# Optimization experiments

Hardware: AMD Instinct MI355X
Metric: run time of the kernel (lower is better)

The kernel has to match this reference:

```python
import jax, jax.numpy as jnp
import numpy as np

N = 4096; F_IN = 512; H = 512; NH = 4; DH = 128
B = 1024; NCTX = 4; L = 64
NODE_VOCAB = 100000; WORD_VOCAB = 32000
ALPHA = 0.2
NEG = -9e15


def setup_inputs() -> dict:
    key = jax.random.key(0)
    ks = jax.random.split(key, 32)
    d = {}
    d['in_nodes'] = jax.random.randint(ks[0], (N,), 0, NODE_VOCAB, dtype=jnp.int32)
    d['out_nodes'] = jax.random.randint(ks[1], (N,), 0, NODE_VOCAB, dtype=jnp.int32)
    d['inner_adj'] = jax.random.randint(ks[2], (N, N), 0, 2, dtype=jnp.int32)
    d['outer_adj'] = jax.random.randint(ks[3], (N, N), 0, 2, dtype=jnp.int32)
    d['in_map_hs'] = jax.random.randint(ks[4], (B,), 0, N, dtype=jnp.int32)
    d['in_map_ts'] = jax.random.randint(ks[5], (B,), 0, N, dtype=jnp.int32)
    d['out_map_hs'] = jax.random.randint(ks[6], (B,), 0, N, dtype=jnp.int32)
    d['out_map_ts'] = jax.random.randint(ks[7], (B,), 0, N, dtype=jnp.int32)
    d['in_ctx'] = jax.random.randint(ks[8], (B * NCTX, L), 0, WORD_VOCAB, dtype=jnp.int32)
    d['in_len'] = jax.random.randint(ks[9], (B * NCTX,), 1, L + 1, dtype=jnp.int32)
    d['out_ctx'] = jax.random.randint(ks[10], (B * NCTX, L), 0, WORD_VOCAB, dtype=jnp.int32)
    d['out_len'] = jax.random.randint(ks[11], (B * NCTX,), 1, L + 1, dtype=jnp.int32)
    d['hs'] = jax.random.randint(ks[12], (B,), 0, NODE_VOCAB, dtype=jnp.int32)
    d['ts'] = jax.random.randint(ks[13], (B,), 0, NODE_VOCAB, dtype=jnp.int32)
    d['node_emb'] = jax.random.normal(ks[14], (NODE_VOCAB, F_IN), jnp.float32) * 0.02
    d['word_emb'] = jax.random.normal(ks[15], (WORD_VOCAB, H), jnp.float32) * 0.02
    d['W_att'] = jax.random.normal(ks[16], (NH, F_IN, DH), jnp.float32) * 0.05
    d['a1'] = jax.random.normal(ks[17], (NH, DH), jnp.float32) * 0.05
    d['a2'] = jax.random.normal(ks[18], (NH, DH), jnp.float32) * 0.05
    d['gru_in_Wi'] = jax.random.normal(ks[19], (3 * H, H), jnp.float32) * 0.04
    d['gru_in_Wh'] = jax.random.normal(ks[20], (3 * H, H), jnp.float32) * 0.04
    d['gru_in_bi'] = jnp.zeros((3 * H,), jnp.float32)
    d['gru_in_bh'] = jnp.zeros((3 * H,), jnp.float32)
    d['gru_out_Wi'] = jax.random.normal(ks[21], (3 * H, H), jnp.float32) * 0.04
    d['gru_out_Wh'] = jax.random.normal(ks[22], (3 * H, H), jnp.float32) * 0.04
    d['gru_out_bi'] = jnp.zeros((3 * H,), jnp.float32)
    d['gru_out_bh'] = jnp.zeros((3 * H,), jnp.float32)
    d['link_W'] = jax.random.normal(ks[23], (2 * H, H), jnp.float32) * 0.03
    d['link_b'] = jnp.zeros((H,), jnp.float32)
    d['gen_W'] = jax.random.normal(ks[24], (2 * H, H), jnp.float32) * 0.03
    d['gen_b'] = jnp.zeros((H,), jnp.float32)
    return d


def gat_multihead(x, adj, W, a1, a2):
    # x: [N, F], W: [NH, F, DH]; all heads vectorized (same math as per-head loop + concat)
    h = jnp.einsum('nf,hfd->hnd', x, W)                      # [NH, N, DH]
    f1 = jnp.einsum('hnd,hd->hn', h, a1)                      # [NH, N]
    f2 = jnp.einsum('hnd,hd->hn', h, a2)                      # [NH, N]
    e = f1[:, :, None] + f2[:, None, :]                       # [NH, N, N]
    e = jnp.where(e > 0, e, ALPHA * e)                        # LeakyReLU(alpha)
    e = jnp.where(adj[None, :, :] > 0, e, NEG)
    att = jax.nn.softmax(e, axis=-1)
    hp = jnp.einsum('hnm,hmd->hnd', att, h)                   # [NH, N, DH]
    return jnp.transpose(hp, (1, 0, 2)).reshape(x.shape[0], -1)  # concat heads: [N, NH*DH]


def gru_last_hidden(x, lengths, Wi, Wh, bi, bh):
    # x: [Bc, T, H]; returns hidden at the last valid timestep (pack_padded semantics)
    T = x.shape[1]
    valid = (jnp.arange(T)[None, :] < lengths[:, None])       # [Bc, T]
    def step(h, inp):
        xt, vt = inp
        gi = xt @ Wi.T + bi
        gh = h @ Wh.T + bh
        ir, iz, inn = jnp.split(gi, 3, axis=1)
        hr, hz, hn = jnp.split(gh, 3, axis=1)
        r = jax.nn.sigmoid(ir + hr)
        z = jax.nn.sigmoid(iz + hz)
        n = jnp.tanh(inn + r * hn)
        h_new = (1 - z) * n + z * h
        return jnp.where(vt[:, None], h_new, h), None
    h0 = jnp.zeros((x.shape[0], Wh.shape[1]), x.dtype)
    hT, _ = jax.lax.scan(step, h0, (jnp.swapaxes(x, 0, 1), valid.T))
    return hT


def reference(in_nodes, out_nodes, inner_adj, outer_adj,
              in_map_hs, in_map_ts, out_map_hs, out_map_ts,
              in_ctx, in_len, out_ctx, out_len, hs, ts,
              node_emb, word_emb, W_att, a1, a2,
              gru_in_Wi, gru_in_Wh, gru_in_bi, gru_in_bh,
              gru_out_Wi, gru_out_Wh, gru_out_bi, gru_out_bh,
              link_W, link_b, gen_W, gen_b):
    # ---- graph_encoder (eval mode: dropout is identity); source uses outer_attentions for both graphs
    out_emb = gat_multihead(node_emb[out_nodes], outer_adj, W_att, a1, a2)
    in_emb = gat_multihead(node_emb[in_nodes], inner_adj, W_att, a1, a2)
    graph_head = jax.nn.elu(in_emb[in_map_hs] + out_emb[out_map_hs])
    graph_tail = jax.nn.elu(in_emb[in_map_ts] + out_emb[out_map_ts])
    # ---- text_encoder, ctx_attn='avg' (returns (out_hidden, in_hidden) order, as in source)
    in_h = gru_last_hidden(word_emb[in_ctx], in_len, gru_in_Wi, gru_in_Wh, gru_in_bi, gru_in_bh)
    out_h = gru_last_hidden(word_emb[out_ctx], out_len, gru_out_Wi, gru_out_Wh, gru_out_bi, gru_out_bh)
    avg_in = jnp.mean(in_h.reshape(-1, NCTX, H), axis=1)
    avg_out = jnp.mean(out_h.reshape(-1, NCTX, H), axis=1)
    text_head, text_tail = avg_out, avg_in
    # ---- integration='concat'
    head = jnp.concatenate([graph_head, text_head], axis=1)
    tail = jnp.concatenate([graph_tail, text_tail], axis=1)
    link_head = head @ link_W + link_b
    link_tail = tail @ link_W + link_b
    gen_head = head @ gen_W + gen_b
    gen_tail = tail @ gen_W + gen_b
    return (link_head, link_tail, gen_head, gen_tail)
```

## Files before the change

### kernel.cpp

```cpp
#include <hip/hip_runtime.h>
#include <stdint.h>


typedef __attribute__((ext_vector_type(8))) short bf16x8;
typedef __attribute__((ext_vector_type(4))) float f32x4;

#define PADW 8

__device__ __forceinline__ unsigned short f2b(float f) {
    union { float f; unsigned int u; } v; v.f = f;
    return (unsigned short)((v.u + 0x7fffu + ((v.u >> 16) & 1u)) >> 16);
}
__device__ __forceinline__ float b2f(unsigned short b) {
    union { unsigned int u; float f; } v; v.u = ((unsigned int)b) << 16;
    return v.f;
}

__global__ void k_prep_wat(const float* watt, unsigned short* dst) {
    int idx = blockIdx.x * 256 + threadIdx.x;
    if (idx >= 512 * 512) return;
    int n = idx >> 9, k = idx & 511;
    int h = n >> 7, d = n & 127;
    dst[idx] = f2b(watt[(h * 512 + k) * 128 + d]);
}

__global__ void k_prep_lg(const float* linkW, const float* genW,
                          unsigned short* dst) {
    int idx = blockIdx.x * 256 + threadIdx.x;
    if (idx >= 2 * 512 * 1024) return;
    int s = idx >> 19;
    int o = idx & 524287;
    int n = o >> 10, k = o & 1023;
    const float* W = s ? genW : linkW;
    dst[idx] = f2b(W[k * 512 + n]);
}

__global__ void k_prep_gruw(const float* a, const float* b, const float* c,
                            const float* d, unsigned short* dst) {
    int idx = blockIdx.x * 256 + threadIdx.x;
    if (idx >= 4 * 786432) return;
    int s = idx / 786432, o = idx % 786432;
    const float* src = (s == 0) ? a : (s == 1) ? b : (s == 2) ? c : d;
    dst[idx] = f2b(src[o]);
}

__global__ void k_prep_whfrag(const float* wh_in, const float* wh_out,
                              unsigned short* dst) {
    int idx = blockIdx.x * 256 + threadIdx.x;
    if (idx >= 2 * 786432) return;
    int g = idx / 786432;
    int r2 = idx % 786432;
    int q = r2 / 262144;
    int r3 = r2 % 262144;
    int nb = r3 >> 15;
    int wn = (r3 >> 14) & 1;
    int nf = (r3 >> 13) & 1;
    int kt = (r3 >> 9) & 15;
    int lane = (r3 >> 3) & 63;
    int e = r3 & 7;
    int row = q * 512 + nb * 64 + wn * 32 + nf * 16 + (lane & 15);
    int col = kt * 32 + (lane >> 4) * 8 + e;
    const float* src = g ? wh_out : wh_in;
    dst[idx] = f2b(src[row * 512 + col]);
}

__global__ void k_prep_wemb(const float* we, unsigned short* dst) {
    int idx = blockIdx.x * 256 + threadIdx.x;
    if (idx >= 2048000) return;
    const float* s = we + (size_t)idx * 8;
    float4 a = ((const float4*)s)[0], b = ((const float4*)s)[1];
    alignas(16) unsigned short t8[8] = {
        f2b(a.x), f2b(a.y), f2b(a.z), f2b(a.w),
        f2b(b.x), f2b(b.y), f2b(b.z), f2b(b.w)};
    *(uint4*)&dst[(size_t)idx * 8] = *(uint4*)t8;
}

__global__ void k_bitpack(const int* inner, const int* outer, unsigned long long* bits) {
    int row = blockIdx.x * 4 + (threadIdx.x >> 6);
    int lane = threadIdx.x & 63;
    int g = row >> 12, i = row & 4095;
    const int* adj = (g ? outer : inner) + (size_t)i * 4096;
    unsigned long long* d = bits + (size_t)row * 64;
    for (int w = 0; w < 64; w++) {
        int v = adj[w * 64 + lane];
        unsigned long long m = __ballot(v != 0);
        if (lane == 0) d[w] = m;
    }
}

__global__ void k_zero(float* hf, unsigned short* hb0) {
    int idx = blockIdx.x * 256 + threadIdx.x;
    if (idx < 8192 * 512) { hf[idx] = 0.f; hb0[idx] = 0; }
}

__global__ void k_sort(const int* in_len, const int* out_len,
                       int* perm, int* slen, int* ipos) {
    int bid = blockIdx.x;
    int half = bid >> 6;
    int v = 64 - (bid & 63);
    const int* len = half ? out_len : in_len;
    int lane = threadIdx.x;
    int base = 0;
    for (int i0 = 0; i0 < 4096; i0 += 64) {
        unsigned long long m = __ballot(len[i0 + lane] > v);
        base += __popcll(m);
    }
    int off = 0;
    for (int i0 = 0; i0 < 4096; i0 += 64) {
        int l = len[i0 + lane];
        unsigned long long m = __ballot(l == v);
        int my = __popcll(m & ((1ull << lane) - 1ull));
        if (l == v) {
            int pos = base + off + my;
            perm[half * 4096 + pos] = i0 + lane;
            slen[half * 4096 + pos] = v;
            ipos[half * 4096 + i0 + lane] = half * 4096 + pos;
        }
        off += __popcll(m);
    }
}

__global__ __launch_bounds__(256) void k_gat_h(
        const unsigned short* Wat, const float* node_emb,
        const int* in_nodes, const int* out_nodes, unsigned short* ht) {
    __shared__ __align__(16) unsigned short At[64][32 + PADW];
    __shared__ __align__(16) unsigned short Bt[64][32 + PADW];
    int nb = blockIdx.x, mb = blockIdx.y, g = blockIdx.z;
    const int* nodes = g ? out_nodes : in_nodes;
    int tid = threadIdx.x, wave = tid >> 6, lane = tid & 63;
    int wn = wave >> 1, wm = wave & 1;
    int r = tid >> 2, seg = (tid & 3) * 8;
    int node = nodes[mb * 64 + r];
    const float* bsrc = node_emb + (size_t)node * 512 + seg;
    const unsigned short* asrc = Wat + (size_t)(nb * 64 + r) * 512 + seg;
    f32x4 z4 = {0.f, 0.f, 0.f, 0.f};
    f32x4 acc[2][2];
#pragma unroll
    for (int a = 0; a < 2; a++)
#pragma unroll
        for (int b = 0; b < 2; b++) acc[a][b] = z4;
    for (int k0 = 0; k0 < 512; k0 += 32) {
        __syncthreads();
        *(uint4*)&At[r][seg] = *(const uint4*)(asrc + k0);
        float4 lo = *(const float4*)(bsrc + k0);
        float4 hi = *(const float4*)(bsrc + k0 + 4);
        alignas(16) unsigned short t8[8] = {
            f2b(lo.x), f2b(lo.y), f2b(lo.z), f2b(lo.w),
            f2b(hi.x), f2b(hi.y), f2b(hi.z), f2b(hi.w)};
        *(uint4*)&Bt[r][seg] = *(uint4*)t8;
        __syncthreads();
#pragma unroll
        for (int nf = 0; nf < 2; nf++) {
            bf16x8 a = *(bf16x8*)&At[wn * 32 + nf * 16 + (lane & 15)][(lane >> 4) * 8];
#pragma unroll
            for (int mf = 0; mf < 2; mf++) {
                bf16x8 b = *(bf16x8*)&Bt[wm * 32 + mf * 16 + (lane & 15)][(lane >> 4) * 8];
                acc[nf][mf] = __builtin_amdgcn_mfma_f32_16x16x32_bf16(a, b, acc[nf][mf], 0, 0, 0);
            }
        }
    }
    unsigned short* htg = ht + (size_t)g * 4 * 128 * 4096;
#pragma unroll
    for (int nf = 0; nf < 2; nf++)
#pragma unroll
        for (int mf = 0; mf < 2; mf++) {
            int i = mb * 64 + wm * 32 + mf * 16 + (lane & 15);
            int n0 = nb * 64 + wn * 32 + nf * 16 + (lane >> 4) * 4;
#pragma unroll
            for (int q = 0; q < 4; q++)
                htg[(size_t)(n0 + q) * 4096 + i] = f2b(acc[nf][mf][q]);
        }
}

__global__ void k_f12(const unsigned short* ht, const float* a1,
                      const float* a2, float* f1, float* f2) {
    int idx = blockIdx.x * 256 + threadIdx.x;
    int i = idx & 4095;
    int h = (idx >> 12) & 3;
    const unsigned short* p = ht + (size_t)(idx >> 12) * 128 * 4096 + i;
    float s1 = 0.f, s2 = 0.f;
    for (int d = 0; d < 128; d++) {
        float v = b2f(p[(size_t)d * 4096]);
        s1 += v * a1[h * 128 + d];
        s2 += v * a2[h * 128 + d];
    }
    f1[idx] = s1; f2[idx] = s2;
}

__global__ __launch_bounds__(256) void k_gat_pv_split2(
        const unsigned short* ht, const unsigned long long* bits,
        const float* f1, const float* f2, float* partO, float* partS) {
    __shared__ __align__(16) unsigned short At[128][64 + PADW];
    __shared__ __align__(16) unsigned short Pt[64][64 + PADW];
    int mb = blockIdx.x, hh = blockIdx.y, g = blockIdx.z;
    int h = hh >> 1, js = hh & 1;
    int tid = threadIdx.x, wave = tid >> 6, lane = tid & 63;
    int wn = wave >> 1, wm = wave & 1;
    const unsigned short* htp = ht + (size_t)(g * 4 + h) * 128 * 4096;
    const float* f2p = f2 + (size_t)(g * 4 + h) * 4096;
    const unsigned long long* bitp = bits + (size_t)g * 4096 * 64 + (size_t)(mb * 64) * 64;
    int iloc = tid >> 2, jc = tid & 3;
    float myf1 = f1[(size_t)(g * 4 + h) * 4096 + mb * 64 + iloc];
    float s_acc = 0.f;
    f32x4 z4 = {0.f, 0.f, 0.f, 0.f};
    f32x4 acc[4][2];
#pragma unroll
    for (int a = 0; a < 4; a++)
#pragma unroll
        for (int b = 0; b < 2; b++) acc[a][b] = z4;
    int pd = tid >> 3, psg = (tid & 7) * 8;
    uint4 apre[4];
#pragma unroll
    for (int q = 0; q < 4; q++)
        apre[q] = *(const uint4*)(htp + (size_t)(pd + q * 32) * 4096 + (js << 11) + psg);
    for (int jt = 0; jt < 32; jt++) {
        int j0 = (js << 11) + (jt << 6);
        __syncthreads();
#pragma unroll
        for (int q = 0; q < 4; q++)
            *(uint4*)&At[pd + q * 32][psg] = apre[q];
        unsigned long long w = bitp[(size_t)iloc * 64 + (j0 >> 6)] >> (jc * 16);
        float fv[16];
#pragma unroll
        for (int q = 0; q < 4; q++) {
            float4 vv = *(const float4*)(f2p + j0 + jc * 16 + q * 4);
            fv[q * 4 + 0] = vv.x; fv[q * 4 + 1] = vv.y;
            fv[q * 4 + 2] = vv.z; fv[q * 4 + 3] = vv.w;
        }
        alignas(16) unsigned short pv[16];
        float rs = 0.f;
#pragma unroll
        for (int e = 0; e < 16; e++) {
            float ee = myf1 + fv[e];
            ee = ee > 0.f ? ee : 0.2f * ee;
            float pval = ((w >> e) & 1ull) ? __expf(ee) : 0.f;
            rs += pval;
            pv[e] = f2b(pval);
        }
        rs += __shfl_xor(rs, 1);
        rs += __shfl_xor(rs, 2);
        s_acc += rs;
        *(uint4*)&Pt[iloc][jc * 16] = *(uint4*)&pv[0];
        *(uint4*)&Pt[iloc][jc * 16 + 8] = *(uint4*)&pv[8];
        __syncthreads();
        if (jt + 1 < 32) {
            int j1 = (js << 11) + ((jt + 1) << 6);
#pragma unroll
            for (int q = 0; q < 4; q++)
                apre[q] = *(const uint4*)(htp + (size_t)(pd + q * 32) * 4096 + j1 + psg);
        }
#pragma unroll
        for (int ks = 0; ks < 2; ks++) {
            bf16x8 bfr[2];
#pragma unroll
            for (int mf = 0; mf < 2; mf++)
                bfr[mf] = *(bf16x8*)&Pt[wm * 32 + mf * 16 + (lane & 15)][ks * 32 + (lane >> 4) * 8];
#pragma unroll
            for (int nf = 0; nf < 4; nf++) {
                bf16x8 a = *(bf16x8*)&At[wn * 64 + nf * 16 + (lane & 15)][ks * 32 + (lane >> 4) * 8];
#pragma unroll
                for (int mf = 0; mf < 2; mf++)
                    acc[nf][mf] = __builtin_amdgcn_mfma_f32_16x16x32_bf16(a, bfr[mf], acc[nf][mf], 0, 0, 0);
            }
        }
    }
    int slab = ((g * 4 + h) * 2 + js);
    if ((tid & 3) == 0)
        partS[(size_t)slab * 4096 + mb * 64 + iloc] = s_acc;
#pragma unroll
    for (int nf = 0; nf < 4; nf++)
#pragma unroll
        for (int mf = 0; mf < 2; mf++) {
            int il = wm * 32 + mf * 16 + (lane & 15);
            int i = mb * 64 + il;
            int d0 = wn * 64 + nf * 16 + (lane >> 4) * 4;
            float4 v;
            v.x = acc[nf][mf][0];
            v.y = acc[nf][mf][1];
            v.z = acc[nf][mf][2];
            v.w = acc[nf][mf][3];
            *(float4*)&partO[((size_t)slab * 4096 + i) * 128 + d0] = v;
        }
}

__global__ void k_pv_combine(const float* partO, const float* partS, float* emb) {
    int idx = blockIdx.x * 256 + threadIdx.x;
    int d = idx & 127;
    int i = (idx >> 7) & 4095;
    int h = (idx >> 19) & 3;
    int g = idx >> 21;
    float s = 0.f, v = 0.f;
#pragma unroll
    for (int js = 0; js < 2; js++) {
        int slab = (g * 4 + h) * 2 + js;
        s += partS[(size_t)slab * 4096 + i];
        v += partO[((size_t)slab * 4096 + i) * 128 + d];
    }
    emb[((size_t)g * 4096 + i) * 512 + h * 128 + d] = s > 0.f ? v / s : 0.f;
}

__global__ __launch_bounds__(256) void k_gat_pv_full(
        const unsigned short* ht, const unsigned long long* bits,
        const float* f1, const float* f2, float* emb) {
    __shared__ __align__(16) unsigned short At[128][64 + PADW];
    __shared__ __align__(16) unsigned short Pt[64][64 + PADW];
    __shared__ float s_lds[64];
    int mb = blockIdx.x, h = blockIdx.y, g = blockIdx.z;
    int tid = threadIdx.x, wave = tid >> 6, lane = tid & 63;
    int wn = wave >> 1, wm = wave & 1;
    const unsigned short* htp = ht + (size_t)(g * 4 + h) * 128 * 4096;
    const float* f2p = f2 + (size_t)(g * 4 + h) * 4096;
    const unsigned long long* bitp = bits + (size_t)g * 4096 * 64 + (size_t)(mb * 64) * 64;
    int iloc = tid >> 2, jc = tid & 3;
    float myf1 = f1[(size_t)(g * 4 + h) * 4096 + mb * 64 + iloc];
    float s_acc = 0.f;
    f32x4 z4 = {0.f, 0.f, 0.f, 0.f};
    f32x4 acc[4][2];
#pragma unroll
    for (int a = 0; a < 4; a++)
#pragma unroll
        for (int b = 0; b < 2; b++) acc[a][b] = z4;
    for (int j0 = 0; j0 < 4096; j0 += 64) {
        __syncthreads();
#pragma unroll
        for (int q = 0; q < 4; q++) {
            int c = tid + q * 256;
            int d = c >> 3, sg = (c & 7) * 8;
            *(uint4*)&At[d][sg] = *(const uint4*)(htp + (size_t)d * 4096 + j0 + sg);
        }
        unsigned long long w = bitp[(size_t)iloc * 64 + (j0 >> 6)] >> (jc * 16);
        float fv[16];
#pragma unroll
        for (int q = 0; q < 4; q++) {
            float4 vv = *(const float4*)(f2p + j0 + jc * 16 + q * 4);
            fv[q * 4 + 0] = vv.x; fv[q * 4 + 1] = vv.y;
            fv[q * 4 + 2] = vv.z; fv[q * 4 + 3] = vv.w;
        }
        alignas(16) unsigned short pv[16];
        float rs = 0.f;
#pragma unroll
        for (int e = 0; e < 16; e++) {
            float ee = myf1 + fv[e];
            ee = ee > 0.f ? ee : 0.2f * ee;
            float pval = ((w >> e) & 1ull) ? __expf(ee) : 0.f;
            rs += pval;
            pv[e] = f2b(pval);
        }
        rs += __shfl_xor(rs, 1);
        rs += __shfl_xor(rs, 2);
        s_acc += rs;
        *(uint4*)&Pt[iloc][jc * 16] = *(uint4*)&pv[0];
        *(uint4*)&Pt[iloc][jc * 16 + 8] = *(uint4*)&pv[8];
        __syncthreads();
#pragma unroll
        for (int ks = 0; ks < 2; ks++) {
            bf16x8 bfr[2];
#pragma unroll
            for (int mf = 0; mf < 2; mf++)
                bfr[mf] = *(bf16x8*)&Pt[wm * 32 + mf * 16 + (lane & 15)][ks * 32 + (lane >> 4) * 8];
#pragma unroll
            for (int nf = 0; nf < 4; nf++) {
                bf16x8 a = *(bf16x8*)&At[wn * 64 + nf * 16 + (lane & 15)][ks * 32 + (lane >> 4) * 8];
#pragma unroll
                for (int mf = 0; mf < 2; mf++)
                    acc[nf][mf] = __builtin_amdgcn_mfma_f32_16x16x32_bf16(a, bfr[mf], acc[nf][mf], 0, 0, 0);
            }
        }
    }
    if ((tid & 3) == 0) s_lds[iloc] = s_acc;
    __syncthreads();
    float* embp = emb + (size_t)g * 4096 * 512;
#pragma unroll
    for (int nf = 0; nf < 4; nf++)
#pragma unroll
        for (int mf = 0; mf < 2; mf++) {
            int il = wm * 32 + mf * 16 + (lane & 15);
            float sv = s_lds[il];
            float inv = sv > 0.f ? 1.f / sv : 0.f;
            int i = mb * 64 + il;
            int d0 = wn * 64 + nf * 16 + (lane >> 4) * 4;
            float4 v;
            v.x = acc[nf][mf][0] * inv;
            v.y = acc[nf][mf][1] * inv;
            v.z = acc[nf][mf][2] * inv;
            v.w = acc[nf][mf][3] * inv;
            *(float4*)&embp[(size_t)i * 512 + h * 128 + d0] = v;
        }
}

__global__ void k_headtail(const float* emb, const int* imh, const int* omh,
                           const int* imt, const int* omt, unsigned short* hcat) {
    int idx = blockIdx.x * 256 + threadIdx.x;
    if (idx >= 2 * 1024 * 512) return;
    int which = idx >> 19;
    int o = idx & 524287;
    int b = o >> 9, c = o & 511;
    int i0 = which ? imt[b] : imh[b];
    int i1 = which ? omt[b] : omh[b];
    float v = emb[(size_t)i0 * 512 + c] + emb[(size_t)(4096 + i1) * 512 + c];
    v = v > 0.f ? v : (__expf(v) - 1.f);
    hcat[(size_t)which * 1024 * 1024 + (size_t)b * 1024 + c] = f2b(v);
}

__global__ __launch_bounds__(256) void k_gi2(
        const unsigned short* wz, const float* word_emb,
        const unsigned short* wemb16, int use16, unsigned short* giTab) {
    __shared__ __align__(16) unsigned short At[128][32 + PADW];
    __shared__ __align__(16) unsigned short Bt[128][32 + PADW];
    int b = blockIdx.x;
    int xcd = b & 7, s = b >> 3;
    int nb = s % 12;
    int wbg = xcd * 63 + s / 12;
    if (wbg >= 500) return;
    int wb = wbg >> 1, g = wbg & 1;
    const unsigned short* Wi = wz + (size_t)(g ? 2 : 0) * 786432;
    int tid = threadIdx.x, wave = tid >> 6, lane = tid & 63;
    int wn = wave >> 1, wm = wave & 1;
    int r = tid >> 1, h2 = tid & 1;
    const unsigned short* asrc = Wi + (size_t)(nb * 128 + r) * 512 + h2 * 16;
    const unsigned short* bsrc16 = wemb16 + (size_t)(wb * 128 + r) * 512 + h2 * 16;
    const float* bsrc32 = word_emb + (size_t)(wb * 128 + r) * 512 + h2 * 16;
    f32x4 z4 = {0.f, 0.f, 0.f, 0.f};
    f32x4 acc[4][4];
#pragma unroll
    for (int a = 0; a < 4; a++)
#pragma unroll
        for (int c = 0; c < 4; c++) acc[a][c] = z4;
    uint4 apre0, apre1, bpre0, bpre1;
    float4 fp0, fp1, fp2v, fp3;
    apre0 = ((const uint4*)asrc)[0];
    apre1 = *(const uint4*)(asrc + 8);
    if (use16) {
        bpre0 = ((const uint4*)bsrc16)[0];
        bpre1 = *(const uint4*)(bsrc16 + 8);
    } else {
        fp0 = ((const float4*)bsrc32)[0]; fp1 = ((const float4*)bsrc32)[1];
        fp2v = ((const float4*)bsrc32)[2]; fp3 = ((const float4*)bsrc32)[3];
    }
    for (int k0 = 0; k0 < 512; k0 += 32) {
        __syncthreads();
        *(uint4*)&At[r][h2 * 16]     = apre0;
        *(uint4*)&At[r][h2 * 16 + 8] = apre1;
        if (use16) {
            *(uint4*)&Bt[r][h2 * 16]     = bpre0;
            *(uint4*)&Bt[r][h2 * 16 + 8] = bpre1;
        } else {
            alignas(16) unsigned short t16[16] = {
                f2b(fp0.x), f2b(fp0.y), f2b(fp0.z), f2b(fp0.w),
                f2b(fp1.x), f2b(fp1.y), f2b(fp1.z), f2b(fp1.w),
                f2b(fp2v.x), f2b(fp2v.y), f2b(fp2v.z), f2b(fp2v.w),
                f2b(fp3.x), f2b(fp3.y), f2b(fp3.z), f2b(fp3.w)};
            *(uint4*)&Bt[r][h2 * 16]     = ((uint4*)t16)[0];
            *(uint4*)&Bt[r][h2 * 16 + 8] = ((uint4*)t16)[1];
        }
        __syncthreads();
        if (k0 + 32 < 512) {
            int k1 = k0 + 32;
            apre0 = *(const uint4*)(asrc + k1);
            apre1 = *(const uint4*)(asrc + k1 + 8);
            if (use16) {
                bpre0 = *(const uint4*)(bsrc16 + k1);
                bpre1 = *(const uint4*)(bsrc16 + k1 + 8);
            } else {
                fp0 = ((const float4*)(bsrc32 + k1))[0];
                fp1 = ((const float4*)(bsrc32 + k1))[1];
                fp2v = ((const float4*)(bsrc32 + k1))[2];
                fp3 = ((const float4*)(bsrc32 + k1))[3];
            }
        }
        bf16x8 av[4], bv[4];
#pragma unroll
        for (int nf = 0; nf < 4; nf++)
            av[nf] = *(bf16x8*)&At[wn * 64 + nf * 16 + (lane & 15)][(lane >> 4) * 8];
#pragma unroll
        for (int mf = 0; mf < 4; mf++)
            bv[mf] = *(bf16x8*)&Bt[wm * 64 + mf * 16 + (lane & 15)][(lane >> 4) * 8];
#pragma unroll
        for (int nf = 0; nf < 4; nf++)
#pragma unroll
            for (int mf = 0; mf < 4; mf++)
                acc[nf][mf] = __builtin_amdgcn_mfma_f32_16x16x32_bf16(av[nf], bv[mf], acc[nf][mf], 0, 0, 0);
    }
#pragma unroll
    for (int nf = 0; nf < 4; nf++)
#pragma unroll
        for (int mf = 0; mf < 4; mf++) {
            int w = wb * 128 + wm * 64 + mf * 16 + (lane & 15);
            int n0 = nb * 128 + wn * 64 + nf * 16 + (lane >> 4) * 4;
            alignas(8) unsigned short o4[4];
#pragma unroll
            for (int q = 0; q < 4; q++) o4[q] = f2b(acc[nf][mf][q]);
            *(unsigned long long*)&giTab[((size_t)g * 32000 + w) * 1536 + n0] =
                *(unsigned long long*)o4;
        }
}

__global__ __launch_bounds__(256) void k_gru_step6(
        const unsigned short* wswz, const unsigned short* giTab,
        const float* bi_in, const float* bh_in,
        const float* bi_out, const float* bh_out,
        const int* in_ctx, const int* out_ctx,
        const int* perm, const int* slen,
        const unsigned short* hb_prev, unsigned short* hb_next, float* hf,
        int t) {
    int b = blockIdx.x;
    int xcd = b & 7, s = b >> 3;
    int nb = s & 7;
    int mb = (s >> 3) * 8 + xcd;
    int p0 = mb * 32;
    if (t >= slen[p0]) return;
    __shared__ __align__(16) unsigned short Ht[32][512 + PADW];
    __shared__ int widx_s[32];
    __shared__ int slen_s[32];
    int tid = threadIdx.x, wave = tid >> 6, lane = tid & 63;
    int wn2 = wave >> 1, nf2 = wave & 1;
    int gsel = mb >= 128;
    const int* ctx = gsel ? out_ctx : in_ctx;
    if (tid < 32) {
        int p = p0 + tid;
        int orig = perm[p];
        widx_s[tid] = ctx[orig * 64 + t];
        slen_s[tid] = slen[p];
    }
    const unsigned short* hbase = hb_prev + (size_t)p0 * 512;
#pragma unroll
    for (int j = 0; j < 8; j++) {
        int flat = tid + j * 256;
        int row = flat >> 6, c16 = flat & 63;
        *(uint4*)&Ht[row][c16 * 8] = *(const uint4*)(hbase + (size_t)row * 512 + c16 * 8);
    }
    __syncthreads();
    const unsigned short* giG = giTab + (size_t)(gsel ? 32000 : 0) * 1536;
    int colbase = nb * 64 + wn2 * 32 + nf2 * 16 + (lane >> 4) * 4;
    unsigned long long gv0[2], gv1[2], gv2[2];
    float4 hold[2];
    bool validf[2];
#pragma unroll
    for (int mf = 0; mf < 2; mf++) {
        int rloc = mf * 16 + (lane & 15);
        validf[mf] = t < slen_s[rloc];
        int w = widx_s[rloc];
        const unsigned short* grow = giG + (size_t)w * 1536;
        hold[mf] = *(const float4*)&hf[(size_t)(p0 + rloc) * 512 + colbase];
        if (validf[mf]) {
            gv0[mf] = __builtin_nontemporal_load((const unsigned long long*)(grow + colbase));
            gv1[mf] = __builtin_nontemporal_load((const unsigned long long*)(grow + 512 + colbase));
            gv2[mf] = __builtin_nontemporal_load((const unsigned long long*)(grow + 1024 + colbase));
        } else {
            gv0[mf] = 0ull; gv1[mf] = 0ull; gv2[mf] = 0ull;
        }
    }
    const unsigned short* wf = wswz + (size_t)gsel * 786432 + nb * 32768
                               + wn2 * 16384 + nf2 * 8192 + (size_t)lane * 8;
    f32x4 z4 = {0.f, 0.f, 0.f, 0.f};
    f32x4 acc[3][2];
#pragma unroll
    for (int a = 0; a < 3; a++)
#pragma unroll
        for (int c = 0; c < 2; c++) acc[a][c] = z4;
#pragma unroll
    for (int kt = 0; kt < 16; kt++) {
        bf16x8 hbv[2];
#pragma unroll
        for (int mf = 0; mf < 2; mf++)
            hbv[mf] = *(bf16x8*)&Ht[mf * 16 + (lane & 15)][kt * 32 + (lane >> 4) * 8];
#pragma unroll
        for (int q = 0; q < 3; q++) {
            bf16x8 a = *(const bf16x8*)(wf + q * 262144 + kt * 512);
#pragma unroll
            for (int mf = 0; mf < 2; mf++)
                acc[q][mf] = __builtin_amdgcn_mfma_f32_16x16x32_bf16(a, hbv[mf], acc[q][mf], 0, 0, 0);
        }
    }
    const float* bi = gsel ? bi_out : bi_in;
    const float* bh = gsel ? bh_out : bh_in;
#pragma unroll
    for (int mf = 0; mf < 2; mf++) {
        int rloc = mf * 16 + (lane & 15);
        int m = p0 + rloc;
        bool valid = validf[mf];
        float ho[4] = {hold[mf].x, hold[mf].y, hold[mf].z, hold[mf].w};
        float hn[4];
        alignas(8) unsigned short hb16[4];
#pragma unroll
        for (int q = 0; q < 4; q++) {
            int n = colbase + q;
            float gir = b2f((unsigned short)(gv0[mf] >> (16 * q)));
            float giz = b2f((unsigned short)(gv1[mf] >> (16 * q)));
            float gin = b2f((unsigned short)(gv2[mf] >> (16 * q)));
            float gr = gir + bi[n] + acc[0][mf][q] + bh[n];
            float gz = giz + bi[512 + n] + acc[1][mf][q] + bh[512 + n];
            float gn = gin + bi[1024 + n];
            float ghn = acc[2][mf][q] + bh[1024 + n];
            float rr = 1.f / (1.f + __expf(-gr));
            float zz = 1.f / (1.f + __expf(-gz));
            float narg = gn + rr * ghn;
            float e2 = __expf(2.f * narg);
            float nn = 1.f - 2.f / (e2 + 1.f);
            float hv = valid ? ((1.f - zz) * nn + zz * ho[q]) : ho[q];
            hn[q] = hv;
            hb16[q] = f2b(hv);
        }
        if (valid)
            *(float4*)&hf[(size_t)m * 512 + colbase] = make_float4(hn[0], hn[1], hn[2], hn[3]);
        *(unsigned long long*)&hb_next[(size_t)m * 512 + colbase] = *(unsigned long long*)hb16;
    }
}

__global__ __launch_bounds__(256) void k_gru_step_fused(
        const unsigned short* wz,
        const float* bi_in, const float* bh_in,
        const float* bi_out, const float* bh_out,
        const int* in_ctx, const int* out_ctx,
        const int* in_len, const int* out_len,
        const float* word_emb,
        const unsigned short* hb_prev, unsigned short* hb_next, float* hf,
        int t) {
    __shared__ __align__(16) unsigned short Wt[6][64][32 + PADW];
    __shared__ __align__(16) unsigned short Xt[64][32 + PADW];
    __shared__ __align__(16) unsigned short Ht[64][32 + PADW];
    int nb = blockIdx.x, mb = blockIdx.y;
    int tid = threadIdx.x, wave = tid >> 6, lane = tid & 63;
    int wn = wave >> 1, wm = wave & 1;
    int gsel = mb >= 64;
    const unsigned short* Wi = wz + (size_t)(gsel ? 2 : 0) * 786432;
    const unsigned short* Wh = wz + (size_t)(gsel ? 3 : 1) * 786432;
    const int* ctx = gsel ? out_ctx : in_ctx;
    int r = tid >> 2, seg = (tid & 3) * 8;
    int mrow = mb * 64 + r;
    int lrow = mrow - (gsel ? 4096 : 0);
    int widx = ctx[lrow * 64 + t];
    const float* xsrc = word_emb + (size_t)widx * 512 + seg;
    const unsigned short* hsrc = hb_prev + (size_t)mrow * 512 + seg;
    f32x4 z4 = {0.f, 0.f, 0.f, 0.f};
    f32x4 acc[6][2][2];
#pragma unroll
    for (int a = 0; a < 6; a++)
#pragma unroll
        for (int b = 0; b < 2; b++)
#pragma unroll
            for (int c = 0; c < 2; c++) acc[a][b][c] = z4;
    for (int k0 = 0; k0 < 512; k0 += 32) {
        __syncthreads();
#pragma unroll
        for (int q = 0; q < 6; q++) {
            const unsigned short* base = (q < 3) ? Wi : Wh;
            int gg = (q < 3) ? q : q - 3;
            *(uint4*)&Wt[q][r][seg] =
                *(const uint4*)(base + (size_t)(gg * 512 + nb * 64 + r) * 512 + k0 + seg);
        }
        float4 xlo = *(const float4*)(xsrc + k0);
        float4 xhi = *(const float4*)(xsrc + k0 + 4);
        alignas(16) unsigned short x8[8] = {
            f2b(xlo.x), f2b(xlo.y), f2b(xlo.z), f2b(xlo.w),
            f2b(xhi.x), f2b(xhi.y), f2b(xhi.z), f2b(xhi.w)};
        *(uint4*)&Xt[r][seg] = *(uint4*)x8;
        *(uint4*)&Ht[r][seg] = *(const uint4*)(hsrc + k0);
        __syncthreads();
        bf16x8 xb[2], hbv[2];
#pragma unroll
        for (int mf = 0; mf < 2; mf++) {
            xb[mf] = *(bf16x8*)&Xt[wm * 32 + mf * 16 + (lane & 15)][(lane >> 4) * 8];
            hbv[mf] = *(bf16x8*)&Ht[wm * 32 + mf * 16 + (lane & 15)][(lane >> 4) * 8];
        }
#pragma unroll
        for (int q = 0; q < 3; q++) {
#pragma unroll
            for (int nf = 0; nf < 2; nf++) {
                bf16x8 ai = *(bf16x8*)&Wt[q][wn * 32 + nf * 16 + (lane & 15)][(lane >> 4) * 8];
                bf16x8 ah = *(bf16x8*)&Wt[q + 3][wn * 32 + nf * 16 + (lane & 15)][(lane >> 4) * 8];
#pragma unroll
                for (int mf = 0; mf < 2; mf++) {
                    acc[q][nf][mf] = __builtin_amdgcn_mfma_f32_16x16x32_bf16(ai, xb[mf], acc[q][nf][mf], 0, 0, 0);
                    acc[q + 3][nf][mf] = __builtin_amdgcn_mfma_f32_16x16x32_bf16(ah, hbv[mf], acc[q + 3][nf][mf], 0, 0, 0);
                }
            }
        }
    }
    const float* bi = gsel ? bi_out : bi_in;
    const float* bh = gsel ? bh_out : bh_in;
    const int* len = gsel ? out_len : in_len;
#pragma unroll
    for (int nf = 0; nf < 2; nf++)
#pragma unroll
        for (int mf = 0; mf < 2; mf++) {
            int m = mb * 64 + wm * 32 + mf * 16 + (lane & 15);
            int lm = m - (gsel ? 4096 : 0);
            int n0 = nb * 64 + wn * 32 + nf * 16 + (lane >> 4) * 4;
            bool valid = t < len[lm];
            float4 hold4 = *(const float4*)&hf[(size_t)m * 512 + n0];
            float ho[4] = {hold4.x, hold4.y, hold4.z, hold4.w};
            float hn[4];
            alignas(8) unsigned short hb16[4];
#pragma unroll
            for (int q = 0; q < 4; q++) {
                int n = n0 + q;
                float gr = acc[0][nf][mf][q] + bi[n] + acc[3][nf][mf][q] + bh[n];
                float gz = acc[1][nf][mf][q] + bi[512 + n] + acc[4][nf][mf][q] + bh[512 + n];
                float gn = acc[2][nf][mf][q] + bi[1024 + n];
                float ghn = acc[5][nf][mf][q] + bh[1024 + n];
                float rr = 1.f / (1.f + __expf(-gr));
                float zz = 1.f / (1.f + __expf(-gz));
                float narg = gn + rr * ghn;
                float e2 = __expf(2.f * narg);
                float nn = 1.f - 2.f / (e2 + 1.f);
                float hv = valid ? ((1.f - zz) * nn + zz * ho[q]) : ho[q];
                hn[q] = hv;
                hb16[q] = f2b(hv);
            }
            *(float4*)&hf[(size_t)m * 512 + n0] = make_float4(hn[0], hn[1], hn[2], hn[3]);
            *(unsigned long long*)&hb_next[(size_t)m * 512 + n0] = *(unsigned long long*)hb16;
        }
}

__global__ void k_avgcat2(const float* hf, const int* ipos, unsigned short* hcat) {
    int idx = blockIdx.x * 256 + threadIdx.x;
    if (idx >= 1024 * 512) return;
    int b = idx >> 9, c = idx & 511;
    float si = 0.f, so = 0.f;
#pragma unroll
    for (int cc = 0; cc < 4; cc++) {
        si += hf[(size_t)ipos[b * 4 + cc] * 512 + c];
        so += hf[(size_t)ipos[4096 + b * 4 + cc] * 512 + c];
    }
    hcat[(size_t)b * 1024 + 512 + c] = f2b(so * 0.25f);
    hcat[(size_t)1024 * 1024 + (size_t)b * 1024 + 512 + c] = f2b(si * 0.25f);
}

__global__ void k_avgcat(const float* hf, unsigned short* hcat) {
    int idx = blockIdx.x * 256 + threadIdx.x;
    if (idx >= 1024 * 512) return;
    int b = idx >> 9, c = idx & 511;
    float si = 0.f, so = 0.f;
#pragma unroll
    for (int cc = 0; cc < 4; cc++) {
        si += hf[(size_t)(b * 4 + cc) * 512 + c];
        so += hf[(size_t)(4096 + b * 4 + cc) * 512 + c];
    }
    hcat[(size_t)b * 1024 + 512 + c] = f2b(so * 0.25f);
    hcat[(size_t)1024 * 1024 + (size_t)b * 1024 + 512 + c] = f2b(si * 0.25f);
}

__global__ __launch_bounds__(256) void k_final(
        const unsigned short* lgT, const unsigned short* hcat,
        const float* link_b, const float* gen_b, float* out) {
    __shared__ __align__(16) unsigned short At[64][32 + PADW];
    __shared__ __align__(16) unsigned short Bt[64][32 + PADW];
    int nb = blockIdx.x, mb = blockIdx.y, z = blockIdx.z;
    int wsel = z >> 1, asel = z & 1;
    const unsigned short* W = lgT + (size_t)wsel * 512 * 1024;
    const unsigned short* A = hcat + (size_t)asel * 1024 * 1024;
    const float* bias = wsel ? gen_b : link_b;
    int tid = threadIdx.x, wave = tid >> 6, lane = tid & 63;
    int wn = wave >> 1, wm = wave & 1;
    int r = tid >> 2, seg = (tid & 3) * 8;
    f32x4 z4 = {0.f, 0.f, 0.f, 0.f};
    f32x4 acc[2][2];
#pragma unroll
    for (int a = 0; a < 2; a++)
#pragma unroll
        for (int b = 0; b < 2; b++) acc[a][b] = z4;
    for (int k0 = 0; k0 < 1024; k0 += 32) {
        __syncthreads();
        *(uint4*)&At[r][seg] = *(const uint4*)(W + (size_t)(nb * 64 + r) * 1024 + k0 + seg);
        *(uint4*)&Bt[r][seg] = *(const uint4*)(A + (size_t)(mb * 64 + r) * 1024 + k0 + seg);
        __syncthreads();
#pragma unroll
        for (int nf = 0; nf < 2; nf++) {
            bf16x8 a = *(bf16x8*)&At[wn * 32 + nf * 16 + (lane & 15)][(lane >> 4) * 8];
#pragma unroll
            for (int mf = 0; mf < 2; mf++) {
                bf16x8 b = *(bf16x8*)&Bt[wm * 32 + mf * 16 + (lane & 15)][(lane >> 4) * 8];
                acc[nf][mf] = __builtin_amdgcn_mfma_f32_16x16x32_bf16(a, b, acc[nf][mf], 0, 0, 0);
            }
        }
    }
#pragma unroll
    for (int nf = 0; nf < 2; nf++)
#pragma unroll
        for (int mf = 0; mf < 2; mf++) {
            int m = mb * 64 + wm * 32 + mf * 16 + (lane & 15);
            int n0 = nb * 64 + wn * 32 + nf * 16 + (lane >> 4) * 4;
            float4 v;
            v.x = acc[nf][mf][0] + bias[n0 + 0];
            v.y = acc[nf][mf][1] + bias[n0 + 1];
            v.z = acc[nf][mf][2] + bias[n0 + 2];
            v.w = acc[nf][mf][3] + bias[n0 + 3];
            *(float4*)&out[(size_t)z * 524288 + (size_t)m * 512 + n0] = v;
        }
}

extern "C" void kernel_launch(void* const* d_in, const int* in_sizes, int n_in,
                              void* d_out, int out_size, void* d_ws, size_t ws_size,
                              hipStream_t stream) {
    const int* in_nodes   = (const int*)d_in[0];
    const int* out_nodes  = (const int*)d_in[1];
    const int* inner_adj  = (const int*)d_in[2];
    const int* outer_adj  = (const int*)d_in[3];
    const int* in_map_hs  = (const int*)d_in[4];
    const int* in_map_ts  = (const int*)d_in[5];
    const int* out_map_hs = (const int*)d_in[6];
    const int* out_map_ts = (const int*)d_in[7];
    const int* in_ctx     = (const int*)d_in[8];
    const int* in_len     = (const int*)d_in[9];
    const int* out_ctx    = (const int*)d_in[10];
    const int* out_len    = (const int*)d_in[11];
    const float* node_emb = (const float*)d_in[14];
    const float* word_emb = (const float*)d_in[15];
    const float* W_att    = (const float*)d_in[16];
    const float* a1       = (const float*)d_in[17];
    const float* a2       = (const float*)d_in[18];
    const float* gi_Wi    = (const float*)d_in[19];
    const float* gi_Wh    = (const float*)d_in[20];
    const float* gi_bi    = (const float*)d_in[21];
    const float* gi_bh    = (const float*)d_in[22];
    const float* go_Wi    = (const float*)d_in[23];
    const float* go_Wh    = (const float*)d_in[24];
    const float* go_bi    = (const float*)d_in[25];
    const float* go_bh    = (const float*)d_in[26];
    const float* link_W   = (const float*)d_in[27];
    const float* link_b   = (const float*)d_in[28];
    const float* gen_W    = (const float*)d_in[29];
    const float* gen_b    = (const float*)d_in[30];

    char* p = (char*)d_ws;
    auto alloc = [&](size_t bytes) {
        char* r = p;
        p += (bytes + 255) & ~(size_t)255;
        return r;
    };
    unsigned short*      Wat  = (unsigned short*)alloc((size_t)512 * 512 * 2);
    unsigned short*      lgT  = (unsigned short*)alloc((size_t)2 * 512 * 1024 * 2);
    unsigned short*      wz   = (unsigned short*)alloc((size_t)4 * 786432 * 2);
    unsigned long long*  bits = (unsigned long long*)alloc((size_t)2 * 4096 * 64 * 8);
    unsigned short*      ht   = (unsigned short*)alloc((size_t)2 * 4 * 128 * 4096 * 2);
    float*               f1   = (float*)alloc((size_t)2 * 4 * 4096 * 4);
    float*               f2   = (float*)alloc((size_t)2 * 4 * 4096 * 4);
    float*               emb  = (float*)alloc((size_t)2 * 4096 * 512 * 4);
    float*               hf   = (float*)alloc((size_t)8192 * 512 * 4);
    unsigned short*      hb   = (unsigned short*)alloc((size_t)2 * 8192 * 512 * 2);
    unsigned short*      hcat = (unsigned short*)alloc((size_t)2 * 1024 * 1024 * 2);
    size_t need_base = (size_t)(p - (char*)d_ws);
    unsigned short*      wswz = (unsigned short*)alloc((size_t)2 * 786432 * 2);
    unsigned short*      giTab = (unsigned short*)alloc((size_t)2 * 32000 * 1536 * 2);
    size_t need_main = (size_t)(p - (char*)d_ws);
    unsigned short*      wemb16 = (unsigned short*)alloc((size_t)32000 * 512 * 2);
    size_t need_tierA = (size_t)(p - (char*)d_ws);
    float* partO = (float*)giTab;
    float* partS = (float*)((char*)giTab + (size_t)16 * 4096 * 128 * 4);
    int* perm = (int*)bits;
    int* slen = perm + 8192;
    int* ipos = slen + 8192;

    bool tierA = ws_size >= need_tierA;
    bool tierB = ws_size >= need_main;
    if (!tierB && ws_size < need_base) return;

    k_prep_wat<<<1024, 256, 0, stream>>>(W_att, Wat);
    k_prep_lg<<<4096, 256, 0, stream>>>(link_W, gen_W, lgT);
    k_prep_gruw<<<12288, 256, 0, stream>>>(gi_Wi, gi_Wh, go_Wi, go_Wh, wz);
    k_bitpack<<<2048, 256, 0, stream>>>(inner_adj, outer_adj, bits);
    k_zero<<<16384, 256, 0, stream>>>(hf, hb);
    k_gat_h<<<dim3(8, 64, 2), 256, 0, stream>>>(Wat, node_emb, in_nodes, out_nodes, ht);
    k_f12<<<128, 256, 0, stream>>>(ht, a1, a2, f1, f2);

    if (tierB) {
        k_prep_whfrag<<<6144, 256, 0, stream>>>(gi_Wh, go_Wh, wswz);
        if (tierA) k_prep_wemb<<<8000, 256, 0, stream>>>(word_emb, wemb16);
        k_gat_pv_split2<<<dim3(64, 8, 2), 256, 0, stream>>>(ht, bits, f1, f2, partO, partS);
        k_pv_combine<<<16384, 256, 0, stream>>>(partO, partS, emb);
        k_sort<<<128, 64, 0, stream>>>(in_len, out_len, perm, slen, ipos);
        k_gi2<<<6048, 256, 0, stream>>>(wz, word_emb,
                                        tierA ? wemb16 : (const unsigned short*)nullptr,
                                        tierA ? 1 : 0, giTab);
        k_headtail<<<4096, 256, 0, stream>>>(emb, in_map_hs, out_map_hs, in_map_ts, out_map_ts, hcat);
        for (int t = 0; t < 64; t++) {
            const unsigned short* hp = hb + (size_t)(t & 1) * 8192 * 512;
            unsigned short* hn = hb + (size_t)((t & 1) ^ 1) * 8192 * 512;
            k_gru_step6<<<2048, 256, 0, stream>>>(
                wswz, giTab, gi_bi, gi_bh, go_bi, go_bh,
                in_ctx, out_ctx, perm, slen, hp, hn, hf, t);
        }
        k_avgcat2<<<2048, 256, 0, stream>>>(hf, ipos, hcat);
    } else {
        k_gat_pv_full<<<dim3(64, 4, 2), 256, 0, stream>>>(ht, bits, f1, f2, emb);
        k_headtail<<<4096, 256, 0, stream>>>(emb, in_map_hs, out_map_hs, in_map_ts, out_map_ts, hcat);
        for (int t = 0; t < 64; t++) {
            const unsigned short* hp = hb + (size_t)(t & 1) * 8192 * 512;
            unsigned short* hn = hb + (size_t)((t & 1) ^ 1) * 8192 * 512;
            k_gru_step_fused<<<dim3(8, 128), 256, 0, stream>>>(
                wz, gi_bi, gi_bh, go_bi, go_bh,
                in_ctx, out_ctx, in_len, out_len, word_emb, hp, hn, hf, t);
        }
        k_avgcat<<<2048, 256, 0, stream>>>(hf, hcat);
    }
    k_final<<<dim3(8, 16, 4), 256, 0, stream>>>(lgT, hcat, link_b, gen_b,
                                                (float*)d_out);
}
```

Baseline: 2.288 ms.

## Replace per-timestep GRU launches with a persistent cooperative kernel using grid sync

```diff
diff --git a/kernel.cpp b/kernel.cpp
--- a/kernel.cpp
+++ b/kernel.cpp
@@ -1,5 +1,8 @@
 #include <hip/hip_runtime.h>
+#include <hip/hip_cooperative_groups.h>
 #include <stdint.h>
+
+namespace cg = cooperative_groups;
 
 
 typedef __attribute__((ext_vector_type(8))) short bf16x8;
@@ -493,6 +496,147 @@
             *(unsigned long long*)&giTab[((size_t)g * 32000 + w) * 1536 + n0] =
                 *(unsigned long long*)o4;
         }
+}
+
+__global__ __launch_bounds__(256, 4) void k_gru_coop(
+        const unsigned short* wswz, const unsigned short* giTab,
+        const float* bi_in, const float* bh_in,
+        const float* bi_out, const float* bh_out,
+        const int* in_ctx, const int* out_ctx,
+        const int* perm, const int* slen,
+        unsigned short* hb0, unsigned short* hb1, float* hf) {
+    cg::grid_group grid = cg::this_grid();
+    int b = blockIdx.x;
+    int xcd = b & 7, u = b >> 3;
+    int nb = u & 7;
+    int mbase = (u >> 3) * 8 + xcd;
+    int tid = threadIdx.x, wave = tid >> 6, lane = tid & 63;
+    int wn2 = wave >> 1, nf2 = wave & 1;
+    int colbase = nb * 64 + wn2 * 32 + nf2 * 16 + (lane >> 4) * 4;
+    __shared__ __align__(16) unsigned short Ht[32][512 + PADW];
+    __shared__ int orig_s[2][32];
+    __shared__ int slen_s[2][32];
+    __shared__ int widx_s[32];
+    int p0A = mbase * 32;
+    int p0B = 4096 + mbase * 32;
+    if (tid < 32) {
+        orig_s[0][tid] = perm[p0A + tid]; slen_s[0][tid] = slen[p0A + tid];
+        orig_s[1][tid] = perm[p0B + tid]; slen_s[1][tid] = slen[p0B + tid];
+    }
+    __syncthreads();
+    int smaxA = slen_s[0][0], smaxB = slen_s[1][0];
+    float4 hregA[2], hregB[2];
+#pragma unroll
+    for (int mf = 0; mf < 2; mf++) {
+        hregA[mf] = make_float4(0.f, 0.f, 0.f, 0.f);
+        hregB[mf] = make_float4(0.f, 0.f, 0.f, 0.f);
+    }
+    f32x4 z4 = {0.f, 0.f, 0.f, 0.f};
+    for (int t = 0; t < 64; ++t) {
+        const unsigned short* hp = (t & 1) ? hb1 : hb0;
+        unsigned short* hn = (t & 1) ? hb0 : hb1;
+#pragma unroll
+        for (int tile = 0; tile < 2; ++tile) {
+            int smax = tile ? smaxB : smaxA;
+            if (t < smax) {
+                int p0 = tile ? p0B : p0A;
+                const int* ctx = tile ? out_ctx : in_ctx;
+                __syncthreads();
+                const unsigned short* hbase = hp + (size_t)p0 * 512;
+#pragma unroll
+                for (int j = 0; j < 8; j++) {
+                    int flat = tid + j * 256;
+                    int row = flat >> 6, c16 = flat & 63;
+                    *(uint4*)&Ht[row][c16 * 8] =
+                        *(const uint4*)(hbase + (size_t)row * 512 + c16 * 8);
+                }
+                if (tid < 32)
+                    widx_s[tid] = ctx[orig_s[tile][tid] * 64 + t];
+                __syncthreads();
+                const unsigned short* giG = giTab + (size_t)(tile ? 32000 : 0) * 1536;
+                unsigned long long gv0[2], gv1[2], gv2[2];
+                bool validf[2];
+#pragma unroll
+                for (int mf = 0; mf < 2; mf++) {
+                    int rloc = mf * 16 + (lane & 15);
+                    validf[mf] = t < slen_s[tile][rloc];
+                    int w = widx_s[rloc];
+                    const unsigned short* grow = giG + (size_t)w * 1536;
+                    if (validf[mf]) {
+                        gv0[mf] = __builtin_nontemporal_load((const unsigned long long*)(grow + colbase));
+                        gv1[mf] = __builtin_nontemporal_load((const unsigned long long*)(grow + 512 + colbase));
+                        gv2[mf] = __builtin_nontemporal_load((const unsigned long long*)(grow + 1024 + colbase));
+                    } else {
+                        gv0[mf] = 0ull; gv1[mf] = 0ull; gv2[mf] = 0ull;
+                    }
+                }
+                const unsigned short* wf = wswz + (size_t)tile * 786432 + nb * 32768
+                                           + wn2 * 16384 + nf2 * 8192 + (size_t)lane * 8;
+                f32x4 acc[3][2];
+#pragma unroll
+                for (int a = 0; a < 3; a++)
+#pragma unroll
+                    for (int c = 0; c < 2; c++) acc[a][c] = z4;
+#pragma unroll
+                for (int kt = 0; kt < 16; kt++) {
+                    bf16x8 hbv[2];
+#pragma unroll
+                    for (int mf = 0; mf < 2; mf++)
+                        hbv[mf] = *(bf16x8*)&Ht[mf * 16 + (lane & 15)][kt * 32 + (lane >> 4) * 8];
+#pragma unroll
+                    for (int q = 0; q < 3; q++) {
+                        bf16x8 a = *(const bf16x8*)(wf + q * 262144 + kt * 512);
+#pragma unroll
+                        for (int mf = 0; mf < 2; mf++)
+                            acc[q][mf] = __builtin_amdgcn_mfma_f32_16x16x32_bf16(a, hbv[mf], acc[q][mf], 0, 0, 0);
+                    }
+                }
+                const float* bi = tile ? bi_out : bi_in;
+                const float* bh = tile ? bh_out : bh_in;
+#pragma unroll
+                for (int mf = 0; mf < 2; mf++) {
+                    int rloc = mf * 16 + (lane & 15);
+                    int m = p0 + rloc;
+                    bool valid = validf[mf];
+                    float4 hold4 = tile ? hregB[mf] : hregA[mf];
+                    float ho[4] = {hold4.x, hold4.y, hold4.z, hold4.w};
+                    float hv4[4];
+                    alignas(8) unsigned short hb16[4];
+#pragma unroll
+                    for (int q = 0; q < 4; q++) {
+                        int n = colbase + q;
+                        float gir = b2f((unsigned short)(gv0[mf] >> (16 * q)));
+                        float giz = b2f((unsigned short)(gv1[mf] >> (16 * q)));
+                        float gin = b2f((unsigned short)(gv2[mf] >> (16 * q)));
+                        float gr = gir + bi[n] + acc[0][mf][q] + bh[n];
+                        float gz = giz + bi[512 + n] + acc[1][mf][q] + bh[512 + n];
+                        float gn = gin + bi[1024 + n];
+                        float ghn = acc[2][mf][q] + bh[1024 + n];
+                        float rr = 1.f / (1.f + __expf(-gr));
+                        float zz = 1.f / (1.f + __expf(-gz));
+                        float narg = gn + rr * ghn;
+                        float e2 = __expf(2.f * narg);
+                        float nn = 1.f - 2.f / (e2 + 1.f);
+                        float hv = valid ? ((1.f - zz) * nn + zz * ho[q]) : ho[q];
+                        hv4[q] = hv;
+                        hb16[q] = f2b(hv);
+                    }
+                    float4 nh = make_float4(hv4[0], hv4[1], hv4[2], hv4[3]);
+                    if (tile) hregB[mf] = nh; else hregA[mf] = nh;
+                    *(unsigned long long*)&hn[(size_t)m * 512 + colbase] =
+                        *(unsigned long long*)hb16;
+                }
+            }
+        }
+        grid.sync();
+    }
+#pragma unroll
+    for (int mf = 0; mf < 2; mf++) {
+        int mA = p0A + mf * 16 + (lane & 15);
+        int mB = p0B + mf * 16 + (lane & 15);
+        *(float4*)&hf[(size_t)mA * 512 + colbase] = hregA[mf];
+        *(float4*)&hf[(size_t)mB * 512 + colbase] = hregB[mf];
+    }
 }
 
 __global__ __launch_bounds__(256) void k_gru_step6(
@@ -874,12 +1018,36 @@
                                         tierA ? wemb16 : (const unsigned short*)nullptr,
                                         tierA ? 1 : 0, giTab);
         k_headtail<<<4096, 256, 0, stream>>>(emb, in_map_hs, out_map_hs, in_map_ts, out_map_ts, hcat);
-        for (int t = 0; t < 64; t++) {
-            const unsigned short* hp = hb + (size_t)(t & 1) * 8192 * 512;
-            unsigned short* hn = hb + (size_t)((t & 1) ^ 1) * 8192 * 512;
-            k_gru_step6<<<2048, 256, 0, stream>>>(
-                wswz, giTab, gi_bi, gi_bh, go_bi, go_bh,
-                in_ctx, out_ctx, perm, slen, hp, hn, hf, t);
+
+        unsigned short* hb0p = hb;
+        unsigned short* hb1p = hb + (size_t)8192 * 512;
+        int maxb = 0;
+        hipError_t oe = hipOccupancyMaxActiveBlocksPerMultiprocessor(
+            &maxb, (const void*)k_gru_coop, 256, 0);
+        bool coop = (oe == hipSuccess && maxb >= 4);
+        if (coop) {
+            const unsigned short* wswz_c = wswz;
+            const unsigned short* giTab_c = giTab;
+            const int* perm_c = perm;
+            const int* slen_c = slen;
+            void* kargs[] = {
+                (void*)&wswz_c, (void*)&giTab_c,
+                (void*)&gi_bi, (void*)&gi_bh, (void*)&go_bi, (void*)&go_bh,
+                (void*)&in_ctx, (void*)&out_ctx,
+                (void*)&perm_c, (void*)&slen_c,
+                (void*)&hb0p, (void*)&hb1p, (void*)&hf};
+            hipError_t le = hipLaunchCooperativeKernel(
+                (const void*)k_gru_coop, dim3(1024), dim3(256), kargs, 0, stream);
+            if (le != hipSuccess) coop = false;
+        }
+        if (!coop) {
+            for (int t = 0; t < 64; t++) {
+                const unsigned short* hp = hb + (size_t)(t & 1) * 8192 * 512;
+                unsigned short* hn = hb + (size_t)((t & 1) ^ 1) * 8192 * 512;
+                k_gru_step6<<<2048, 256, 0, stream>>>(
+                    wswz, giTab, gi_bi, gi_bh, go_bi, go_bh,
+                    in_ctx, out_ctx, perm, slen, hp, hn, hf, t);
+            }
         }
         k_avgcat2<<<2048, 256, 0, stream>>>(hf, ipos, hcat);
     } else {
```

After: 2.285 ms. No clear change (-0.1%).
